# Performance work log

Hardware: AMD Instinct MI355X
Metric: run time of the kernel (lower is better)

Reference implementation:

```python
import jax, jax.numpy as jnp
import numpy as np

NUM_ITERATIONS = 3
EPS = 1e-12


def _squash(s):
    # s: (..., V). squash(s) = |s|^2 * s / ((1+|s|^2) * |s|)
    sq = jnp.sum(s * s, axis=-1, keepdims=True)
    return sq * s / ((1.0 + sq) * jnp.sqrt(sq))


def setup_inputs() -> dict:
    key = jax.random.key(0)
    kx, kw = jax.random.split(key)
    B, L, P, V, Q = 16, 64, 1024, 64, 16
    x = jax.random.normal(kx, (B, P, Q), dtype=jnp.float32)
    W = 0.01 * jax.random.normal(kw, (L, P, V, Q), dtype=jnp.float32)
    return {"x": x, "W": W}


def reference(x, W):
    # u_hat[b,l,p,v] = sum_q W[l,p,v,q] * x[b,p,q]
    u_hat = jnp.einsum('lpvq,bpq->blpv', W, x)  # (B, L, P, V)
    B, L, P, V = u_hat.shape
    b_ij = jnp.zeros((B, L, P), dtype=u_hat.dtype)
    c_ij = None
    v = None
    for it in range(NUM_ITERATIONS):  # small fixed unroll
        c_ij = jax.nn.softmax(b_ij, axis=1)  # softmax over latent caps
        s = jnp.einsum('blp,blpv->blv', c_ij, u_hat)
        v = _squash(s)  # (B, L, V)
        if it < NUM_ITERATIONS - 1:
            # agreement update: b_ij += <v_j, u_hat>
            b_ij = b_ij + jnp.einsum('blv,blpv->blp', v, u_hat)
    # T-score: coupling entropy over latent axis, per primary capsule
    cT = jnp.swapaxes(c_ij, 1, 2)  # (B, P, L)
    entropy = -jnp.sum(cT * jnp.log(cT + EPS), axis=-1)  # (B, P)
    T = jnp.mean(1.0 - entropy / np.log(float(L)))
    # D-score: max over caps of population std (over batch) of activation norms
    v_norm = jnp.linalg.norm(v, axis=-1)  # (B, L)
    D = jnp.max(jnp.std(v_norm, axis=0))
    return v, T, D
```

## Files before the change

### kernel.cpp

```cpp
#include <hip/hip_runtime.h>
#include <hip/hip_bf16.h>

#define B 16
#define L 64
#define P 1024
#define V 64
#define Q 16
#define LN64 4.158883083359672f

#define CHBC 16
#define NCH_BC (P / CHBC)
#define LPV ((size_t)L * P * V)

typedef unsigned short ushort8_t __attribute__((ext_vector_type(8)));
typedef __attribute__((ext_vector_type(8))) short bf16x8;
typedef __attribute__((ext_vector_type(4))) float f32x4;

typedef const __attribute__((address_space(1))) void* gld_gptr_t;
typedef __attribute__((address_space(3))) void* gld_lptr_t;

static __device__ __forceinline__ float bf2f(ushort u) {
    return __uint_as_float(((unsigned int)u) << 16);
}
static __device__ __forceinline__ ushort f2bf(float f) {
    unsigned int x = __float_as_uint(f);
    unsigned int r = (x + 0x7fffu + ((x >> 16) & 1u)) >> 16;
    return (ushort)r;
}
static __device__ __forceinline__ unsigned pk2(float lo, float hi) {
    return (unsigned)f2bf(lo) | ((unsigned)f2bf(hi) << 16);
}

static __device__ __forceinline__ float wsum64(float v) {
#pragma unroll
    for (int m = 32; m > 0; m >>= 1) v += __shfl_xor(v, m, 64);
    return v;
}
static __device__ __forceinline__ float wmax64(float v) {
#pragma unroll
    for (int m = 32; m > 0; m >>= 1) v = fmaxf(v, __shfl_xor(v, m, 64));
    return v;
}

union FragU { uint4 u; bf16x8 s; };

__global__ __launch_bounds__(256, 3) void k_uhat(const float* __restrict__ Wt,
                                                 const float* __restrict__ x,
                                                 ushort* __restrict__ uhat,
                                                 float* __restrict__ sp0) {
    const int t = threadIdx.x;
    const int w = t >> 6;
    const int lane = t & 63;
    const int kb = lane >> 4;
    const int cc = lane & 15;
    const int ch = blockIdx.x;
    const int l = blockIdx.y;
    const int p0 = ch * 32;

    __shared__ __align__(16) char smem[49152];
    unsigned int* xstage = (unsigned int*)smem;

#pragma unroll
    for (int i = 0; i < 16; ++i) {
        const int e = i * 256 + t;
        const int pp = e >> 7, ln = (e >> 2) & 31, m = e & 3;
        const int b = ln & 15, qb = (ln >> 4) * 8;
        const float2 xv = *reinterpret_cast<const float2*>(
            x + ((size_t)b * P + p0 + pp) * Q + qb + 2 * m);
        xstage[e] = pk2(xv.x, xv.y);
    }
    __syncthreads();

    uint4 af[8];
#pragma unroll
    for (int i = 0; i < 8; ++i) {
        if (lane < 32)
            af[i] = *reinterpret_cast<const uint4*>(
                smem + ((size_t)(w * 8 + i) * 32 + lane) * 16);
        else
            af[i] = (uint4){0u, 0u, 0u, 0u};
    }
    __syncthreads();

    char* ring = smem + w * 12288;
    const int sperm = (lane & ~3) | ((lane & 3) ^ ((lane >> 3) & 3));
    const char* gW = (const char*)(Wt + ((size_t)l * P + p0 + w * 8) * (V * Q))
                     + (size_t)sperm * 16;
    const int xk = (cc >> 1) & 3;

    f32x4 cacc0 = {0.f, 0.f, 0.f, 0.f}, cacc1 = {0.f, 0.f, 0.f, 0.f};
    f32x4 cacc2 = {0.f, 0.f, 0.f, 0.f}, cacc3 = {0.f, 0.f, 0.f, 0.f};

#define STAGE(i_)                                                             \
    {                                                                         \
        const char* s_ = gW + (size_t)(i_) * 4096;                            \
        char* d_ = ring + ((i_) % 3) * 4096;                                  \
        __builtin_amdgcn_global_load_lds((gld_gptr_t)(s_ + 0),                \
                                         (gld_lptr_t)(d_ + 0), 16, 0, 0);     \
        __builtin_amdgcn_global_load_lds((gld_gptr_t)(s_ + 1024),             \
                                         (gld_lptr_t)(d_ + 1024), 16, 0, 0);  \
        __builtin_amdgcn_global_load_lds((gld_gptr_t)(s_ + 2048),             \
                                         (gld_lptr_t)(d_ + 2048), 16, 0, 0);  \
        __builtin_amdgcn_global_load_lds((gld_gptr_t)(s_ + 3072),             \
                                         (gld_lptr_t)(d_ + 3072), 16, 0, 0);  \
    }

#define BFRAG(g_, dst_)                                                       \
    {                                                                         \
        if (lane < 32) {                                                      \
            const char* rb_ = ring + (slot_) * 4096 + (cc + 16 * (g_)) * 64;  \
            const float4 f0 =                                                 \
                *(const float4*)(rb_ + (((2 * kb + 0) ^ xk) << 4));           \
            const float4 f1 =                                                 \
                *(const float4*)(rb_ + (((2 * kb + 1) ^ xk) << 4));           \
            dst_.u = (uint4){pk2(f0.x, f0.y), pk2(f0.z, f0.w),                \
                             pk2(f1.x, f1.y), pk2(f1.z, f1.w)};               \
        } else {                                                              \
            dst_.u = (uint4){0u, 0u, 0u, 0u};                                 \
        }                                                                     \
    }

#define MMGROUP(g_, cacc_)                                                    \
    {                                                                         \
        FragU bf_;                                                            \
        BFRAG(g_, bf_);                                                       \
        f32x4 d_ = __builtin_amdgcn_mfma_f32_16x16x32_bf16(afr.s, bf_.s,      \
                                                           cacc_, 0, 0, 0);   \
        f32x4 u_ = d_ - cacc_;                                                \
        cacc_ = d_;                                                           \
        const unsigned lo01_ = pk2(u_[0], u_[1]);                             \
        const unsigned lo23_ = pk2(u_[2], u_[3]);                             \
        ushort* up_ = ub_ + (g_) * 16;                                        \
        up_[0] = (ushort)lo01_;                                               \
        up_[LPV] = (ushort)(lo01_ >> 16);                                     \
        up_[2 * LPV] = (ushort)lo23_;                                         \
        up_[3 * LPV] = (ushort)(lo23_ >> 16);                                 \
    }

#define COMPUTE(i_)                                                           \
    {                                                                         \
        const int slot_ = (i_) % 3;                                           \
        const int p_ = p0 + w * 8 + (i_);                                     \
        FragU afr; afr.u = af[i_];                                            \
        ushort* ub_ = uhat +                                                  \
            (((size_t)(kb * 4) * L + l) * P + p_) * V + cc;                   \
        MMGROUP(0, cacc0);                                                    \
        MMGROUP(1, cacc1);                                                    \
        MMGROUP(2, cacc2);                                                    \
        MMGROUP(3, cacc3);                                                    \
    }

#define WAITV(N)                                                              \
    asm volatile("s_waitcnt vmcnt(" #N ")" ::: "memory");                     \
    __builtin_amdgcn_sched_barrier(0);

    STAGE(0); STAGE(1);
    WAITV(4);  STAGE(2); COMPUTE(0);
    WAITV(16); STAGE(3); COMPUTE(1);
    WAITV(32); STAGE(4); COMPUTE(2);
    WAITV(32); STAGE(5); COMPUTE(3);
    WAITV(32); STAGE(6); COMPUTE(4);
    WAITV(32); STAGE(7); COMPUTE(5);
    WAITV(32); COMPUTE(6);
    WAITV(28); COMPUTE(7);

    {
        float* sb = sp0 + (((size_t)l * 128 + ch * 4 + w) * 16) * 64;
#pragma unroll
        for (int i2 = 0; i2 < 4; ++i2) {
            const int b = kb * 4 + i2;
            sb[(size_t)b * 64 + cc + 0]  = cacc0[i2];
            sb[(size_t)b * 64 + cc + 16] = cacc1[i2];
            sb[(size_t)b * 64 + cc + 32] = cacc2[i2];
            sb[(size_t)b * 64 + cc + 48] = cacc3[i2];
        }
    }
#undef STAGE
#undef BFRAG
#undef MMGROUP
#undef COMPUTE
#undef WAITV
}

__global__ __launch_bounds__(256) void k_v(const float* __restrict__ sp,
                                           size_t cb, size_t cl, size_t cs,
                                           int nch, float scale,
                                           float* __restrict__ vout,
                                           float* __restrict__ norms) {
    const int b = blockIdx.y;
    const int w = threadIdx.x >> 6, lane = threadIdx.x & 63;
    const int l = blockIdx.x * 4 + w;
    const float* p = sp + cb * b + cl * l + lane;
    float s = 0.f;
#pragma unroll 8
    for (int ch = 0; ch < nch; ++ch) s += p[(size_t)ch * cs];
    s *= scale;
    float sq = wsum64(s * s);
    float f = sqrtf(sq) / (1.0f + sq);
    vout[((size_t)b * L + l) * V + lane] = s * f;
    if (norms && lane == 0) norms[b * L + l] = sq / (1.0f + sq);
}

__global__ __launch_bounds__(512, 4) void k_bc(const ushort* __restrict__ uhat,
                                               const float* __restrict__ vv,
                                               float* __restrict__ bbuf,
                                               float* __restrict__ sp,
                                               float* __restrict__ Tsum,
                                               int add_prev, int do_T) {
    const int ch = blockIdx.x, b = blockIdx.y;
    const int p0 = ch * CHBC;
    const int t = threadIdx.x;
    const int w = t >> 6, lane = t & 63;
    const int pl8 = lane >> 3;
    const int vg8 = lane & 7;
    const int l0 = w * 8;

    __shared__ float vsh[L][V];
    __shared__ float bl[CHBC][L + 1];
    __shared__ float twv[8];

    {
        const float4* vvp = reinterpret_cast<const float4*>(vv + (size_t)b * L * V);
        float4* vshp = reinterpret_cast<float4*>(&vsh[0][0]);
#pragma unroll
        for (int i = 0; i < 2; ++i) vshp[t + i * 512] = vvp[t + i * 512];
    }

    ushort8_t ur[8][2];
    {
        const ushort* ubase = uhat + (((size_t)(b * L + l0)) * P + p0 + pl8) * V + vg8 * 8;
#pragma unroll
        for (int li = 0; li < 8; ++li) {
#pragma unroll
            for (int ph = 0; ph < 2; ++ph)
                ur[li][ph] = *reinterpret_cast<const ushort8_t*>(
                    ubase + ((size_t)li * P + ph * 8) * V);
        }
    }
    __syncthreads();

#pragma unroll
    for (int li = 0; li < 8; ++li) {
        const int l = l0 + li;
        const float4 va = *reinterpret_cast<const float4*>(&vsh[l][vg8 * 8]);
        const float4 vb = *reinterpret_cast<const float4*>(&vsh[l][vg8 * 8 + 4]);
#pragma unroll
        for (int ph = 0; ph < 2; ++ph) {
            float d;
            d = bf2f(ur[li][ph][0]) * va.x;
            d = fmaf(bf2f(ur[li][ph][1]), va.y, d);
            d = fmaf(bf2f(ur[li][ph][2]), va.z, d);
            d = fmaf(bf2f(ur[li][ph][3]), va.w, d);
            d = fmaf(bf2f(ur[li][ph][4]), vb.x, d);
            d = fmaf(bf2f(ur[li][ph][5]), vb.y, d);
            d = fmaf(bf2f(ur[li][ph][6]), vb.z, d);
            d = fmaf(bf2f(ur[li][ph][7]), vb.w, d);
            d += __shfl_xor(d, 1, 64);
            d += __shfl_xor(d, 2, 64);
            d += __shfl_xor(d, 4, 64);
            if (vg8 == 0) bl[ph * 8 + pl8][l] = d;
        }
    }
    __syncthreads();

    float tloc = 0.f;
#pragma unroll
    for (int pi = 0; pi < 2; ++pi) {
        const int pli = w * 2 + pi;
        const int p = p0 + pli;
        float bv = bl[pli][lane];
        float* bp = bbuf + ((size_t)b * P + p) * L;
        if (add_prev) bv += bp[lane];
        bp[lane] = bv;
        float m = wmax64(bv);
        float e = __expf(bv - m);
        float ssum = wsum64(e);
        float cc = e / ssum;
        bl[pli][lane] = cc;
        if (do_T) tloc += cc * __logf(64.0f * (cc + 1e-12f));
    }
    if (do_T) {
        float dsum = wsum64(tloc);
        if (lane == 0) twv[w] = dsum;
    }
    __syncthreads();
    if (do_T && t == 0) {
        float s8 = twv[0] + twv[1] + twv[2] + twv[3] +
                   twv[4] + twv[5] + twv[6] + twv[7];
        atomicAdd(Tsum, s8 * (1.0f / LN64));
    }

    float* spb = sp + (size_t)(b * NCH_BC + ch) * L * V;
#pragma unroll
    for (int li = 0; li < 8; ++li) {
        const int l = l0 + li;
        const float cA = bl[pl8][l];
        const float cB = bl[8 + pl8][l];
        float4 pa, pb;
        pa.x = cA * bf2f(ur[li][0][0]) + cB * bf2f(ur[li][1][0]);
        pa.y = cA * bf2f(ur[li][0][1]) + cB * bf2f(ur[li][1][1]);
        pa.z = cA * bf2f(ur[li][0][2]) + cB * bf2f(ur[li][1][2]);
        pa.w = cA * bf2f(ur[li][0][3]) + cB * bf2f(ur[li][1][3]);
        pb.x = cA * bf2f(ur[li][0][4]) + cB * bf2f(ur[li][1][4]);
        pb.y = cA * bf2f(ur[li][0][5]) + cB * bf2f(ur[li][1][5]);
        pb.z = cA * bf2f(ur[li][0][6]) + cB * bf2f(ur[li][1][6]);
        pb.w = cA * bf2f(ur[li][0][7]) + cB * bf2f(ur[li][1][7]);
#pragma unroll
        for (int m = 8; m <= 32; m <<= 1) {
            pa.x += __shfl_xor(pa.x, m, 64);
            pa.y += __shfl_xor(pa.y, m, 64);
            pa.z += __shfl_xor(pa.z, m, 64);
            pa.w += __shfl_xor(pa.w, m, 64);
            pb.x += __shfl_xor(pb.x, m, 64);
            pb.y += __shfl_xor(pb.y, m, 64);
            pb.z += __shfl_xor(pb.z, m, 64);
            pb.w += __shfl_xor(pb.w, m, 64);
        }
        if (pl8 == 0) {
            *reinterpret_cast<float4*>(spb + (size_t)l * V + vg8 * 8) = pa;
            *reinterpret_cast<float4*>(spb + (size_t)l * V + vg8 * 8 + 4) = pb;
        }
    }
}

__global__ void k_final(const float* __restrict__ Tsum,
                        const float* __restrict__ norms,
                        float* __restrict__ out) {
    const int lane = threadIdx.x & 63;
    float n[B];
    float sum = 0.f;
#pragma unroll
    for (int b = 0; b < B; ++b) { n[b] = norms[b * L + lane]; sum += n[b]; }
    const float mean = sum * (1.0f / B);
    float var = 0.f;
#pragma unroll
    for (int b = 0; b < B; ++b) { float d = n[b] - mean; var = fmaf(d, d, var); }
    var *= (1.0f / B);
    float sd = sqrtf(var);
    float D = wmax64(sd);
    if (lane == 0) {
        out[B * L * V] = Tsum[0] * (1.0f / (B * P));
        out[B * L * V + 1] = D;
    }
}

extern "C" void kernel_launch(void* const* d_in, const int* in_sizes, int n_in,
                              void* d_out, int out_size, void* d_ws, size_t ws_size,
                              hipStream_t stream) {
    const float* x = (const float*)d_in[0];
    const float* W = (const float*)d_in[1];
    float* out = (float*)d_out;

    char* ws = (char*)d_ws;
    ushort* uhat = (ushort*)ws;
    size_t off = (size_t)B * L * P * V * 2;
    float* spbuf = (float*)(ws + off);
    off += (size_t)64 * 128 * 16 * 64 * 4;
    float* vbuf  = (float*)(ws + off); off += (size_t)B * L * V * 4;
    float* bbuf  = (float*)(ws + off); off += (size_t)B * P * L * 4;
    float* norms = (float*)(ws + off); off += (size_t)B * L * 4;
    float* Tsum  = (float*)(ws + off); off += 256;

    hipMemsetAsync(Tsum, 0, sizeof(float), stream);

    hipLaunchKernelGGL(k_uhat, dim3(32, 64), dim3(256), 0, stream, W, x, uhat, spbuf);
    hipLaunchKernelGGL(k_v, dim3(L / 4, B), dim3(256), 0, stream,
                       spbuf, (size_t)64, (size_t)131072, (size_t)1024, 128,
                       1.0f / 64.0f, vbuf, (float*)nullptr);
    hipLaunchKernelGGL(k_bc, dim3(NCH_BC, B), dim3(512), 0, stream,
                       uhat, vbuf, bbuf, spbuf, Tsum, 0, 0);
    hipLaunchKernelGGL(k_v, dim3(L / 4, B), dim3(256), 0, stream,
                       spbuf, (size_t)NCH_BC * L * V, (size_t)V, (size_t)L * V,
                       NCH_BC, 1.0f, vbuf, (float*)nullptr);
    hipLaunchKernelGGL(k_bc, dim3(NCH_BC, B), dim3(512), 0, stream,
                       uhat, vbuf, bbuf, spbuf, Tsum, 1, 1);
    hipLaunchKernelGGL(k_v, dim3(L / 4, B), dim3(256), 0, stream,
                       spbuf, (size_t)NCH_BC * L * V, (size_t)V, (size_t)L * V,
                       NCH_BC, 1.0f, out, norms);
    hipLaunchKernelGGL(k_final, dim3(1), dim3(64), 0, stream, Tsum, norms, out);
}
```

Baseline: 241.7 us.

## Swap MFMA operands and store u_hat in a batch-inner permuted layout

The u_hat MFMA now takes W as the A operand and x as the B operand. Each lane holds consecutive batch entries, so u_hat can be written as two 16-byte vector stores into an (L,P,B,V) layout with a permuted V order, replacing scattered 2-byte stores. The partial-sum stores become float4 writes, and the vmcnt waits are lowered to match the smaller number of outstanding stores. k_bc reads the new layout, and the final k_v un-permutes the V index on output. This adds layout bookkeeping, and correctness depends on the permutation being consistent across every kernel.

```diff
diff --git a/kernel.cpp b/kernel.cpp
--- a/kernel.cpp
+++ b/kernel.cpp
@@ -10,7 +10,6 @@
 
 #define CHBC 16
 #define NCH_BC (P / CHBC)
-#define LPV ((size_t)L * P * V)
 
 typedef unsigned short ushort8_t __attribute__((ext_vector_type(8)));
 typedef __attribute__((ext_vector_type(8))) short bf16x8;
@@ -105,7 +104,7 @@
                                          (gld_lptr_t)(d_ + 3072), 16, 0, 0);  \
     }
 
-#define BFRAG(g_, dst_)                                                       \
+#define WFRAG(g_, dst_)                                                       \
     {                                                                         \
         if (lane < 32) {                                                      \
             const char* rb_ = ring + (slot_) * 4096 + (cc + 16 * (g_)) * 64;  \
@@ -120,34 +119,34 @@
         }                                                                     \
     }
 
-#define MMGROUP(g_, cacc_)                                                    \
+#define MMG(g_, cacc_, u_)                                                    \
     {                                                                         \
-        FragU bf_;                                                            \
-        BFRAG(g_, bf_);                                                       \
-        f32x4 d_ = __builtin_amdgcn_mfma_f32_16x16x32_bf16(afr.s, bf_.s,      \
+        FragU wf_;                                                            \
+        WFRAG(g_, wf_);                                                       \
+        f32x4 d_ = __builtin_amdgcn_mfma_f32_16x16x32_bf16(wf_.s, bx_.s,      \
                                                            cacc_, 0, 0, 0);   \
-        f32x4 u_ = d_ - cacc_;                                                \
+        u_ = d_ - cacc_;                                                      \
         cacc_ = d_;                                                           \
-        const unsigned lo01_ = pk2(u_[0], u_[1]);                             \
-        const unsigned lo23_ = pk2(u_[2], u_[3]);                             \
-        ushort* up_ = ub_ + (g_) * 16;                                        \
-        up_[0] = (ushort)lo01_;                                               \
-        up_[LPV] = (ushort)(lo01_ >> 16);                                     \
-        up_[2 * LPV] = (ushort)lo23_;                                         \
-        up_[3 * LPV] = (ushort)(lo23_ >> 16);                                 \
     }
 
 #define COMPUTE(i_)                                                           \
     {                                                                         \
         const int slot_ = (i_) % 3;                                           \
         const int p_ = p0 + w * 8 + (i_);                                     \
-        FragU afr; afr.u = af[i_];                                            \
-        ushort* ub_ = uhat +                                                  \
-            (((size_t)(kb * 4) * L + l) * P + p_) * V + cc;                   \
-        MMGROUP(0, cacc0);                                                    \
-        MMGROUP(1, cacc1);                                                    \
-        MMGROUP(2, cacc2);                                                    \
-        MMGROUP(3, cacc3);                                                    \
+        FragU bx_; bx_.u = af[i_];                                            \
+        f32x4 u0_, u1_, u2_, u3_;                                             \
+        MMG(0, cacc0, u0_);                                                   \
+        MMG(1, cacc1, u1_);                                                   \
+        MMG(2, cacc2, u2_);                                                   \
+        MMG(3, cacc3, u3_);                                                   \
+        uint4 A_, B_;                                                         \
+        A_.x = pk2(u0_[0], u1_[0]); A_.y = pk2(u2_[0], u3_[0]);               \
+        A_.z = pk2(u0_[1], u1_[1]); A_.w = pk2(u2_[1], u3_[1]);               \
+        B_.x = pk2(u0_[2], u1_[2]); B_.y = pk2(u2_[2], u3_[2]);               \
+        B_.z = pk2(u0_[3], u1_[3]); B_.w = pk2(u2_[3], u3_[3]);               \
+        ushort* ub_ = uhat + (((size_t)l * P + p_) * B + cc) * V + kb * 16;   \
+        *reinterpret_cast<uint4*>(ub_) = A_;                                  \
+        *reinterpret_cast<uint4*>(ub_ + 8) = B_;                              \
     }
 
 #define WAITV(N)                                                              \
@@ -155,36 +154,36 @@
     __builtin_amdgcn_sched_barrier(0);
 
     STAGE(0); STAGE(1);
-    WAITV(4);  STAGE(2); COMPUTE(0);
-    WAITV(16); STAGE(3); COMPUTE(1);
-    WAITV(32); STAGE(4); COMPUTE(2);
-    WAITV(32); STAGE(5); COMPUTE(3);
-    WAITV(32); STAGE(6); COMPUTE(4);
-    WAITV(32); STAGE(7); COMPUTE(5);
-    WAITV(32); COMPUTE(6);
-    WAITV(28); COMPUTE(7);
+    WAITV(2); STAGE(2); COMPUTE(0);
+    WAITV(4); STAGE(3); COMPUTE(1);
+    WAITV(6); STAGE(4); COMPUTE(2);
+    WAITV(6); STAGE(5); COMPUTE(3);
+    WAITV(6); STAGE(6); COMPUTE(4);
+    WAITV(6); STAGE(7); COMPUTE(5);
+    WAITV(6); COMPUTE(6);
+    WAITV(2); COMPUTE(7);
 
     {
-        float* sb = sp0 + (((size_t)l * 128 + ch * 4 + w) * 16) * 64;
-#pragma unroll
-        for (int i2 = 0; i2 < 4; ++i2) {
-            const int b = kb * 4 + i2;
-            sb[(size_t)b * 64 + cc + 0]  = cacc0[i2];
-            sb[(size_t)b * 64 + cc + 16] = cacc1[i2];
-            sb[(size_t)b * 64 + cc + 32] = cacc2[i2];
-            sb[(size_t)b * 64 + cc + 48] = cacc3[i2];
-        }
+        float* sb = sp0 + (((size_t)l * 128 + ch * 4 + w) * 16 + cc) * 64 + kb * 16;
+        float4 q0 = {cacc0[0], cacc1[0], cacc2[0], cacc3[0]};
+        float4 q1 = {cacc0[1], cacc1[1], cacc2[1], cacc3[1]};
+        float4 q2 = {cacc0[2], cacc1[2], cacc2[2], cacc3[2]};
+        float4 q3 = {cacc0[3], cacc1[3], cacc2[3], cacc3[3]};
+        *reinterpret_cast<float4*>(sb + 0) = q0;
+        *reinterpret_cast<float4*>(sb + 4) = q1;
+        *reinterpret_cast<float4*>(sb + 8) = q2;
+        *reinterpret_cast<float4*>(sb + 12) = q3;
     }
 #undef STAGE
-#undef BFRAG
-#undef MMGROUP
+#undef WFRAG
+#undef MMG
 #undef COMPUTE
 #undef WAITV
 }
 
 __global__ __launch_bounds__(256) void k_v(const float* __restrict__ sp,
                                            size_t cb, size_t cl, size_t cs,
-                                           int nch, float scale,
+                                           int nch, float scale, int unperm,
                                            float* __restrict__ vout,
                                            float* __restrict__ norms) {
     const int b = blockIdx.y;
@@ -197,7 +196,9 @@
     s *= scale;
     float sq = wsum64(s * s);
     float f = sqrtf(sq) / (1.0f + sq);
-    vout[((size_t)b * L + l) * V + lane] = s * f;
+    const int vi = unperm ? ((lane & 3) * 16 + (lane >> 4) * 4 + ((lane >> 2) & 3))
+                          : lane;
+    vout[((size_t)b * L + l) * V + vi] = s * f;
     if (norms && lane == 0) norms[b * L + l] = sq / (1.0f + sq);
 }
 
@@ -226,15 +227,16 @@
         for (int i = 0; i < 2; ++i) vshp[t + i * 512] = vvp[t + i * 512];
     }
 
+    const size_t LSTR = (size_t)P * B * V;
     ushort8_t ur[8][2];
     {
-        const ushort* ubase = uhat + (((size_t)(b * L + l0)) * P + p0 + pl8) * V + vg8 * 8;
+        const ushort* ubase = uhat + (((size_t)l0 * P + p0 + pl8) * B + b) * V + vg8 * 8;
 #pragma unroll
         for (int li = 0; li < 8; ++li) {
 #pragma unroll
             for (int ph = 0; ph < 2; ++ph)
                 ur[li][ph] = *reinterpret_cast<const ushort8_t*>(
-                    ubase + ((size_t)li * P + ph * 8) * V);
+                    ubase + (size_t)li * LSTR + (size_t)ph * 8 * B * V);
         }
     }
     __syncthreads();
@@ -366,16 +368,16 @@
     hipLaunchKernelGGL(k_uhat, dim3(32, 64), dim3(256), 0, stream, W, x, uhat, spbuf);
     hipLaunchKernelGGL(k_v, dim3(L / 4, B), dim3(256), 0, stream,
                        spbuf, (size_t)64, (size_t)131072, (size_t)1024, 128,
-                       1.0f / 64.0f, vbuf, (float*)nullptr);
+                       1.0f / 64.0f, 0, vbuf, (float*)nullptr);
     hipLaunchKernelGGL(k_bc, dim3(NCH_BC, B), dim3(512), 0, stream,
                        uhat, vbuf, bbuf, spbuf, Tsum, 0, 0);
     hipLaunchKernelGGL(k_v, dim3(L / 4, B), dim3(256), 0, stream,
                        spbuf, (size_t)NCH_BC * L * V, (size_t)V, (size_t)L * V,
-                       NCH_BC, 1.0f, vbuf, (float*)nullptr);
+                       NCH_BC, 1.0f, 0, vbuf, (float*)nullptr);
     hipLaunchKernelGGL(k_bc, dim3(NCH_BC, B), dim3(512), 0, stream,
                        uhat, vbuf, bbuf, spbuf, Tsum, 1, 1);
     hipLaunchKernelGGL(k_v, dim3(L / 4, B), dim3(256), 0, stream,
                        spbuf, (size_t)NCH_BC * L * V, (size_t)V, (size_t)L * V,
-                       NCH_BC, 1.0f, out, norms);
+                       NCH_BC, 1.0f, 1, out, norms);
     hipLaunchKernelGGL(k_final, dim3(1), dim3(64), 0, stream, Tsum, norms, out);
 }
```

Result: faster. 220.4 us (-8.8%).
